# Optimization experiments

Hardware: AMD Instinct MI355X
Metric: run time of the kernel (lower is better)

## Reference

```python
import jax, jax.numpy as jnp
import numpy as np

N = 300000   # nodes
E = 600000   # edges
H = 128      # hidden_dim
L = 5        # num_layers
G = 8192     # graphs in batch
AV = 128     # atom feature vocab
BV = 8       # bond feature vocab
NAF = 9      # atom int features (OGB)
NBF = 3      # bond int features (OGB)
BN_EPS = 1e-5


def setup_inputs() -> dict:
    key = jax.random.key(0)
    ks = jax.random.split(key, 16)
    s = 0.05
    x = jax.random.randint(ks[0], (N, NAF), 0, 100, dtype=jnp.int32)
    edge_index = jax.random.randint(ks[1], (2, E), 0, N, dtype=jnp.int32)
    edge_attr = jax.random.randint(ks[2], (E, NBF), 0, 6, dtype=jnp.int32)
    batch = jnp.sort(jax.random.randint(ks[3], (N,), 0, G, dtype=jnp.int32))
    atom_emb = jax.random.normal(ks[4], (NAF, AV, H), dtype=jnp.float32) * s
    bond_emb = jax.random.normal(ks[5], (L, NBF, BV, H), dtype=jnp.float32) * s
    eps = jnp.zeros((L,), dtype=jnp.float32)  # GIN train_eps init 0
    w1 = jax.random.normal(ks[6], (L, H, H), dtype=jnp.float32) * s
    b1 = jnp.zeros((L, H), dtype=jnp.float32)
    bn1_g = jnp.ones((L, H), dtype=jnp.float32)
    bn1_b = jnp.zeros((L, H), dtype=jnp.float32)
    w2 = jax.random.normal(ks[7], (L, H, H), dtype=jnp.float32) * s
    b2 = jnp.zeros((L, H), dtype=jnp.float32)
    bn_g = jnp.ones((L, H), dtype=jnp.float32)
    bn_b = jnp.zeros((L, H), dtype=jnp.float32)
    cw1 = jax.random.normal(ks[8], (H, H), dtype=jnp.float32) * s
    cb1 = jnp.zeros((H,), dtype=jnp.float32)
    cw2 = jax.random.normal(ks[9], (H, 1), dtype=jnp.float32) * s
    cb2 = jnp.zeros((1,), dtype=jnp.float32)
    return dict(x=x, edge_index=edge_index, edge_attr=edge_attr, batch=batch,
                atom_emb=atom_emb, bond_emb=bond_emb, eps=eps,
                w1=w1, b1=b1, bn1_g=bn1_g, bn1_b=bn1_b, w2=w2, b2=b2,
                bn_g=bn_g, bn_b=bn_b, cw1=cw1, cb1=cb1, cw2=cw2, cb2=cb2)


def _bn(h, g, b):
    # BatchNorm1d in training mode: biased batch stats over nodes
    mu = h.mean(axis=0)
    var = h.var(axis=0)
    return g * (h - mu) * jax.lax.rsqrt(var + BN_EPS) + b


def reference(x, edge_index, edge_attr, batch, atom_emb, bond_emb, eps,
              w1, b1, bn1_g, bn1_b, w2, b2, bn_g, bn_b, cw1, cb1, cw2, cb2):
    seg = jax.ops.segment_sum
    # AtomEncoder: sum of per-feature embedding lookups -> [N, H]
    h = atom_emb[0][x[:, 0]]
    for f in range(1, NAF):
        h = h + atom_emb[f][x[:, f]]
    row, col = edge_index[0], edge_index[1]
    # in-degree of row used by scatter_reduce_(mean, include_self=True): divide by count+1
    deg = seg(jnp.ones((E,), dtype=h.dtype), row, num_segments=N)
    inv = 1.0 / (deg + 1.0)
    for l in range(L):
        # BondEncoder for this layer -> [E, H]
        be = (bond_emb[l, 0][edge_attr[:, 0]]
              + bond_emb[l, 1][edge_attr[:, 1]]
              + bond_emb[l, 2][edge_attr[:, 2]])
        # scatter mean (include_self=True over initial zeros): sum/(count+1)
        bond_agg = seg(be, row, num_segments=N) * inv[:, None]
        h_in = h + bond_agg
        # GINConv: sum-aggregate source feats at targets, (1+eps)*self + aggr, then MLP
        aggr = seg(h_in[row], col, num_segments=N)
        z = (1.0 + eps[l]) * h_in + aggr
        z = jax.nn.relu(_bn(z @ w1[l] + b1[l], bn1_g[l], bn1_b[l]))
        z = z @ w2[l] + b2[l]
        h = _bn(z, bn_g[l], bn_b[l])
        if l < L - 1:
            h = jax.nn.relu(h)  # dropout p=0 -> identity
    pooled = seg(h, batch, num_segments=G)  # global_add_pool -> [G, H]
    out = jax.nn.relu(pooled @ cw1 + cb1) @ cw2 + cb2  # [G, 1]
    return out.squeeze(-1)
```

## Files before the change

### kernel.cpp

```cpp
#include <hip/hip_runtime.h>
#include <cstdint>

#define NN 300000
#define NE 600000
#define HD 128
#define NL 5
#define NG 8192
#define AVOC 128
#define BVOC 8
#define NAF 9
#define NBF 3
#define BN_EPS 1e-5f

#define SCAN_B 2048
#define SCAN_NB ((NN + SCAN_B - 1) / SCAN_B)

#define G1ROWS 128
#define G1BLK ((NN + G1ROWS - 1) / G1ROWS)
#define GBM 256
#define GBLK ((NN + GBM - 1) / GBM)

typedef unsigned short u16;
typedef unsigned int u32;
typedef __attribute__((ext_vector_type(8))) short bf16x8;
typedef __attribute__((ext_vector_type(4))) float f32x4;

static __device__ __forceinline__ void atomAddF(float* p, float v) { unsafeAtomicAdd(p, v); }

static __device__ __forceinline__ float bf2f(u16 v) {
  union { u32 u; float f; } c; c.u = ((u32)v) << 16; return c.f;
}
static __device__ __forceinline__ u16 f2bf(float f) {
  union { float f; u32 u; } c; c.f = f;
  u32 u = c.u;
  return (u16)((u + 0x7FFFu + ((u >> 16) & 1u)) >> 16);
}
static __device__ __forceinline__ u32 cvtpk(float a, float b) {
  u32 r;
  asm("v_cvt_pk_bf16_f32 %0, %1, %2" : "=v"(r) : "v"(a), "v"(b));
  return r;
}
static __device__ __forceinline__ void unp8(uint4 p, float* v) {
  v[0] = bf2f((u16)(p.x & 0xffff)); v[1] = bf2f((u16)(p.x >> 16));
  v[2] = bf2f((u16)(p.y & 0xffff)); v[3] = bf2f((u16)(p.y >> 16));
  v[4] = bf2f((u16)(p.z & 0xffff)); v[5] = bf2f((u16)(p.z >> 16));
  v[6] = bf2f((u16)(p.w & 0xffff)); v[7] = bf2f((u16)(p.w >> 16));
}
static __device__ __forceinline__ uint4 pk8(const float* v) {
  uint4 p;
  p.x = ((u32)f2bf(v[1]) << 16) | f2bf(v[0]);
  p.y = ((u32)f2bf(v[3]) << 16) | f2bf(v[2]);
  p.z = ((u32)f2bf(v[5]) << 16) | f2bf(v[4]);
  p.w = ((u32)f2bf(v[7]) << 16) | f2bf(v[6]);
  return p;
}

static __device__ __forceinline__ void split8(const float* v, bf16x8& hi, bf16x8& lo) {
  union { u32 u[4]; bf16x8 h; } H, L;
  H.u[0] = cvtpk(v[0], v[1]); H.u[1] = cvtpk(v[2], v[3]);
  H.u[2] = cvtpk(v[4], v[5]); H.u[3] = cvtpk(v[6], v[7]);
  float r[8];
  r[0] = bf2f((u16)(H.u[0] & 0xffff)); r[1] = bf2f((u16)(H.u[0] >> 16));
  r[2] = bf2f((u16)(H.u[1] & 0xffff)); r[3] = bf2f((u16)(H.u[1] >> 16));
  r[4] = bf2f((u16)(H.u[2] & 0xffff)); r[5] = bf2f((u16)(H.u[2] >> 16));
  r[6] = bf2f((u16)(H.u[3] & 0xffff)); r[7] = bf2f((u16)(H.u[3] >> 16));
  L.u[0] = cvtpk(v[0] - r[0], v[1] - r[1]); L.u[1] = cvtpk(v[2] - r[2], v[3] - r[3]);
  L.u[2] = cvtpk(v[4] - r[4], v[5] - r[5]); L.u[3] = cvtpk(v[6] - r[6], v[7] - r[7]);
  hi = H.h; lo = L.h;
}

__global__ __launch_bounds__(256) void count_k(const int* __restrict__ ei,
    int* __restrict__ cnt_row, int* __restrict__ cnt_col) {
  int e = blockIdx.x * 256 + threadIdx.x;
  if (e >= NE) return;
  atomicAdd(&cnt_row[ei[e]], 1);
  atomicAdd(&cnt_col[ei[NE + e]], 1);
}

__global__ __launch_bounds__(256) void scan_block_k(int* __restrict__ P, int* __restrict__ bsum) {
  __shared__ int s[256];
  int b = blockIdx.x, t = threadIdx.x;
  int base = b * SCAN_B + t * 8;
  int v[8]; int ts = 0;
#pragma unroll
  for (int j = 0; j < 8; j++) { v[j] = (base + j < NN) ? P[base + j] : 0; ts += v[j]; }
  s[t] = ts;
  __syncthreads();
  for (int off = 1; off < 256; off <<= 1) {
    int tmp = 0;
    if (t >= off) tmp = s[t - off];
    __syncthreads();
    if (t >= off) s[t] += tmp;
    __syncthreads();
  }
  if (t == 255) bsum[b] = s[255];
  int run = (t == 0) ? 0 : s[t - 1];
#pragma unroll
  for (int j = 0; j < 8; j++) {
    if (base + j < NN) P[base + j] = run;
    run += v[j];
  }
}

__global__ __launch_bounds__(256) void scan_tops_k(int* __restrict__ bsum, int* __restrict__ totOut) {
  __shared__ int s[256];
  int t = threadIdx.x;
  s[t] = (t < SCAN_NB) ? bsum[t] : 0;
  __syncthreads();
  for (int off = 1; off < 256; off <<= 1) {
    int tmp = 0;
    if (t >= off) tmp = s[t - off];
    __syncthreads();
    if (t >= off) s[t] += tmp;
    __syncthreads();
  }
  if (t < SCAN_NB) bsum[t] = (t == 0) ? 0 : s[t - 1];
  if (t == 255) *totOut = s[255];
}

__global__ __launch_bounds__(256) void scan_add_k(int* __restrict__ P, const int* __restrict__ bsum) {
  int b = blockIdx.x, t = threadIdx.x;
  int off = bsum[b];
  int base = b * SCAN_B + t * 8;
#pragma unroll
  for (int j = 0; j < 8; j++)
    if (base + j < NN) P[base + j] += off;
}

__global__ __launch_bounds__(256) void fill_k(const int* __restrict__ ei,
    const int* __restrict__ ea,
    const int* __restrict__ ptr_row, const int* __restrict__ ptr_col,
    int* __restrict__ fillr, int* __restrict__ fillc,
    u16* __restrict__ adjc, int* __restrict__ adj_col) {
  int e = blockIdx.x * 256 + threadIdx.x;
  if (e >= NE) return;
  int r = ei[e], c = ei[NE + e];
  int a0 = ea[e * 3 + 0], a1 = ea[e * 3 + 1], a2 = ea[e * 3 + 2];
  int p1 = atomicAdd(&fillr[r], 1);
  adjc[ptr_row[r] + p1] = (u16)(a0 + (a1 << 3) + (a2 << 6));
  int p2 = atomicAdd(&fillc[c], 1);
  adj_col[ptr_col[c] + p2] = r;
}

__global__ __launch_bounds__(256) void inv_k(const int* __restrict__ ptr_row, float* __restrict__ inv) {
  int n = blockIdx.x * 256 + threadIdx.x;
  if (n < NN) inv[n] = 1.0f / ((float)(ptr_row[n + 1] - ptr_row[n]) + 1.0f);
}

__global__ __launch_bounds__(256) void gp_k(const int* __restrict__ batch, int* __restrict__ gp) {
  int g = blockIdx.x * 256 + threadIdx.x;
  if (g > NG) return;
  int lo = 0, hi = NN;
  while (lo < hi) { int mid = (lo + hi) >> 1; if (batch[mid] < g) lo = mid + 1; else hi = mid; }
  gp[g] = lo;
}

__global__ __launch_bounds__(256) void wsplit_k(const float* __restrict__ w1,
    const float* __restrict__ w2, u16* __restrict__ Wt_hi, u16* __restrict__ Wt_lo) {
  int m = blockIdx.x;
  const float* W = (m < NL) ? (w1 + (size_t)m * HD * HD) : (w2 + (size_t)(m - NL) * HD * HD);
  int t = threadIdx.x;
  for (int p = 0; p < 64; p++) {
    int o = p * 256 + t;
    int c = o >> 7, k = o & 127;
    float w = W[k * HD + c];
    u16 hi = f2bf(w);
    float lo = w - bf2f(hi);
    Wt_hi[(size_t)m * HD * HD + o] = hi;
    Wt_lo[(size_t)m * HD * HD + o] = f2bf(lo);
  }
}

__global__ __launch_bounds__(128) void cmb_k(const float* __restrict__ bond_emb,
    u16* __restrict__ cmb) {
  int b = blockIdx.x;
  int l = b >> 9, c = b & 511;
  int t = threadIdx.x;
  const float* be = bond_emb + (size_t)l * NBF * BVOC * HD;
  float v = be[(c & 7) * HD + t] + be[(BVOC + ((c >> 3) & 7)) * HD + t]
          + be[(2 * BVOC + (c >> 6)) * HD + t];
  cmb[(size_t)b * HD + t] = f2bf(v);
}


template<bool ENC>
__global__ __launch_bounds__(256) void bond_k(
    const u16* __restrict__ cmb, const int* __restrict__ ptr_row,
    const u16* __restrict__ adjc, const float* __restrict__ inv,
    const int* __restrict__ x, const float* __restrict__ emb,
    const u16* __restrict__ Z2, const float* __restrict__ stR,
    const float* __restrict__ bg, const float* __restrict__ bb_,
    u16* __restrict__ A) {
  __shared__ int sx[16 * NAF];
  __shared__ float sss[256];
  int t = threadIdx.x;
  int nb = blockIdx.x * 16;
  int n = nb + (t >> 4);
  int c8 = t & 15;
  if constexpr (ENC) {
    if (t < 16 * NAF && nb * NAF + t < NN * NAF) sx[t] = x[nb * NAF + t];
    __syncthreads();
  } else {
    if (t < 128) {
      float mean = stR[t] * (1.0f / NN);
      float var = stR[128 + t] * (1.0f / NN) - mean * mean;
      float sc = bg[t] * rsqrtf(var + BN_EPS);
      sss[t] = sc;
      sss[128 + t] = fmaf(-mean, sc, bb_[t]);
    }
    __syncthreads();
  }
  if (n >= NN) return;
  int beg = ptr_row[n], end = ptr_row[n + 1];
  float acc[8] = {0.f, 0.f, 0.f, 0.f, 0.f, 0.f, 0.f, 0.f};
  {
    int i = beg;
    int ca = (beg < end) ? (int)adjc[beg] : 0;
    int cb = (beg + 1 < end) ? (int)adjc[beg + 1] : 0;
    while (i + 1 < end) {
      uint4 pa = *(const uint4*)(cmb + ((size_t)ca << 7) + c8 * 8);
      uint4 pb = *(const uint4*)(cmb + ((size_t)cb << 7) + c8 * 8);
      i += 2;
      if (i < end)     ca = (int)adjc[i];
      if (i + 1 < end) cb = (int)adjc[i + 1];
      float va[8], vb[8];
      unp8(pa, va); unp8(pb, vb);
#pragma unroll
      for (int j = 0; j < 8; j++) acc[j] += va[j];
#pragma unroll
      for (int j = 0; j < 8; j++) acc[j] += vb[j];
    }
    if (i < end) {
      uint4 pa = *(const uint4*)(cmb + ((size_t)ca << 7) + c8 * 8);
      float va[8]; unp8(pa, va);
#pragma unroll
      for (int j = 0; j < 8; j++) acc[j] += va[j];
    }
  }
  float h[8];
  if constexpr (ENC) {
#pragma unroll
    for (int j = 0; j < 8; j++) h[j] = 0.f;
#pragma unroll
    for (int f = 0; f < NAF; f++) {
      int v = sx[(t >> 4) * NAF + f];
      const float* e = emb + ((size_t)(f * AVOC + v)) * HD + c8 * 8;
      float4 e0 = *(const float4*)e;
      float4 e1 = *(const float4*)(e + 4);
      h[0] += e0.x; h[1] += e0.y; h[2] += e0.z; h[3] += e0.w;
      h[4] += e1.x; h[5] += e1.y; h[6] += e1.z; h[7] += e1.w;
    }
  } else {
    uint4 p = *(const uint4*)(Z2 + (size_t)n * HD + c8 * 8);
    unp8(p, h);
#pragma unroll
    for (int j = 0; j < 8; j++)
      h[j] = fmaxf(fmaf(h[j], sss[c8 * 8 + j], sss[128 + c8 * 8 + j]), 0.f);
  }
  float iv = inv[n];
#pragma unroll
  for (int j = 0; j < 8; j++) h[j] = fmaf(acc[j], iv, h[j]);
  *(uint4*)(A + (size_t)n * HD + c8 * 8) = pk8(h);
}

__global__ __launch_bounds__(512, 4) void gemm1_aggr_k(
    const u16* __restrict__ A, const int* __restrict__ ptr_col,
    const int* __restrict__ adj_col, const float* __restrict__ eps, int lyr,
    const u16* __restrict__ Whi, const u16* __restrict__ Wlo,
    const float* __restrict__ bias, u16* __restrict__ Z1,
    float* __restrict__ stats) {
  __shared__ u16 sW[2 * HD * HD];
  const int tid = threadIdx.x;
#pragma unroll
  for (int p = 0; p < 4; p++) {
    int idx = tid + p * 512;
    int col = idx >> 4, k16 = idx & 15;
    uint4 vh = *(const uint4*)(Whi + idx * 8);
    uint4 vl = *(const uint4*)(Wlo + idx * 8);
    int so = (col << 7) + ((k16 << 3) ^ ((col & 7) << 3));
    *(uint4*)(sW + so) = vh;
    *(uint4*)(sW + HD * HD + so) = vl;
  }
  __syncthreads();

  const int bswz = (blockIdx.x & 7) * (G1BLK >> 3) + (blockIdx.x >> 3);

  const float se = 1.0f + eps[lyr];
  const int l = tid & 63, w = tid >> 6;
  const int lr = l & 15, lk = l >> 4;
  const int rw = bswz * G1ROWS + w * 16;
  const int gr = rw + lr;
  const int kb0 = lk * 8;

  float z[4][8];
#pragma unroll
  for (int ks = 0; ks < 4; ks++)
#pragma unroll
    for (int j = 0; j < 8; j++) z[ks][j] = 0.f;

  if (gr < NN) {
    const u16* ap = A + (size_t)gr * HD + kb0;
    uint4 s0 = *(const uint4*)(ap);
    uint4 s1 = *(const uint4*)(ap + 32);
    uint4 s2 = *(const uint4*)(ap + 64);
    uint4 s3 = *(const uint4*)(ap + 96);
    int beg = ptr_col[gr], end = ptr_col[gr + 1];
    {
      float v[8];
      unp8(s0, v);
#pragma unroll
      for (int j = 0; j < 8; j++) z[0][j] = v[j] * se;
      unp8(s1, v);
#pragma unroll
      for (int j = 0; j < 8; j++) z[1][j] = v[j] * se;
      unp8(s2, v);
#pragma unroll
      for (int j = 0; j < 8; j++) z[2][j] = v[j] * se;
      unp8(s3, v);
#pragma unroll
      for (int j = 0; j < 8; j++) z[3][j] = v[j] * se;
    }
    int i = beg;
    int srcA = (beg < end) ? adj_col[beg] : 0;
    int srcB = (beg + 1 < end) ? adj_col[beg + 1] : 0;
    while (i + 1 < end) {
      const u16* pa = A + (size_t)srcA * HD + kb0;
      const u16* pb = A + (size_t)srcB * HD + kb0;
      uint4 a0 = *(const uint4*)(pa);
      uint4 a1 = *(const uint4*)(pa + 32);
      uint4 a2 = *(const uint4*)(pa + 64);
      uint4 a3 = *(const uint4*)(pa + 96);
      uint4 b0 = *(const uint4*)(pb);
      uint4 b1 = *(const uint4*)(pb + 32);
      uint4 b2 = *(const uint4*)(pb + 64);
      uint4 b3 = *(const uint4*)(pb + 96);
      i += 2;
      if (i < end)     srcA = adj_col[i];
      if (i + 1 < end) srcB = adj_col[i + 1];
      float u[8];
      unp8(a0, u);
#pragma unroll
      for (int j = 0; j < 8; j++) z[0][j] += u[j];
      unp8(a1, u);
#pragma unroll
      for (int j = 0; j < 8; j++) z[1][j] += u[j];
      unp8(a2, u);
#pragma unroll
      for (int j = 0; j < 8; j++) z[2][j] += u[j];
      unp8(a3, u);
#pragma unroll
      for (int j = 0; j < 8; j++) z[3][j] += u[j];
      unp8(b0, u);
#pragma unroll
      for (int j = 0; j < 8; j++) z[0][j] += u[j];
      unp8(b1, u);
#pragma unroll
      for (int j = 0; j < 8; j++) z[1][j] += u[j];
      unp8(b2, u);
#pragma unroll
      for (int j = 0; j < 8; j++) z[2][j] += u[j];
      unp8(b3, u);
#pragma unroll
      for (int j = 0; j < 8; j++) z[3][j] += u[j];
    }
    if (i < end) {
      const u16* pa = A + (size_t)srcA * HD + kb0;
      uint4 a0 = *(const uint4*)(pa);
      uint4 a1 = *(const uint4*)(pa + 32);
      uint4 a2 = *(const uint4*)(pa + 64);
      uint4 a3 = *(const uint4*)(pa + 96);
      float u[8];
      unp8(a0, u);
#pragma unroll
      for (int j = 0; j < 8; j++) z[0][j] += u[j];
      unp8(a1, u);
#pragma unroll
      for (int j = 0; j < 8; j++) z[1][j] += u[j];
      unp8(a2, u);
#pragma unroll
      for (int j = 0; j < 8; j++) z[2][j] += u[j];
      unp8(a3, u);
#pragma unroll
      for (int j = 0; j < 8; j++) z[3][j] += u[j];
    }
  }

  bf16x8 ah[4], al[4];
#pragma unroll
  for (int ks = 0; ks < 4; ks++) split8(z[ks], ah[ks], al[ks]);

  f32x4 acc[8];
#pragma unroll
  for (int jt = 0; jt < 8; jt++) acc[jt] = (f32x4){0.f, 0.f, 0.f, 0.f};
#pragma unroll
  for (int ks = 0; ks < 4; ks++) {
    const int kb = ks * 32 + kb0;
#pragma unroll
    for (int jt = 0; jt < 8; jt++) {
      int col = jt * 16 + lr;
      int so = (col << 7) + (kb ^ ((col & 7) << 3));
      bf16x8 bh = *(const bf16x8*)(sW + so);
      bf16x8 bl = *(const bf16x8*)(sW + HD * HD + so);
      acc[jt] = __builtin_amdgcn_mfma_f32_16x16x32_bf16(ah[ks], bh, acc[jt], 0, 0, 0);
      acc[jt] = __builtin_amdgcn_mfma_f32_16x16x32_bf16(al[ks], bh, acc[jt], 0, 0, 0);
      acc[jt] = __builtin_amdgcn_mfma_f32_16x16x32_bf16(ah[ks], bl, acc[jt], 0, 0, 0);
    }
  }

  float bb[8];
#pragma unroll
  for (int jt = 0; jt < 8; jt++) bb[jt] = bias[jt * 16 + lr];
  float cs[8], cq[8];
#pragma unroll
  for (int jt = 0; jt < 8; jt++) { cs[jt] = 0.f; cq[jt] = 0.f; }
#pragma unroll
  for (int j = 0; j < 4; j++) {
    int gr2 = rw + lk * 4 + j;
    bool ok = gr2 < NN;
#pragma unroll
    for (int jt = 0; jt < 8; jt++) {
      float o = acc[jt][j] + bb[jt];
      if (ok) { cs[jt] += o; cq[jt] += o * o; }
      float on = __shfl_xor(o, 1);
      u32 pw = cvtpk(o, on);
      if (ok && !(l & 1))
        *(u32*)(Z1 + (size_t)gr2 * HD + jt * 16 + lr) = pw;
    }
  }
#pragma unroll
  for (int jt = 0; jt < 8; jt++) {
    cs[jt] += __shfl_xor(cs[jt], 16); cs[jt] += __shfl_xor(cs[jt], 32);
    cq[jt] += __shfl_xor(cq[jt], 16); cq[jt] += __shfl_xor(cq[jt], 32);
  }
  __syncthreads();
  float* sS = (float*)sW;
  if (lk == 0) {
#pragma unroll
    for (int jt = 0; jt < 8; jt++) {
      sS[w * HD + jt * 16 + lr] = cs[jt];
      sS[1024 + w * HD + jt * 16 + lr] = cq[jt];
    }
  }
  __syncthreads();
  if (tid < HD) {
    float s = 0.f, q = 0.f;
#pragma unroll
    for (int g = 0; g < 8; g++) { s += sS[g * HD + tid]; q += sS[1024 + g * HD + tid]; }
    atomAddF(&stats[tid], s);
    atomAddF(&stats[HD + tid], q);
  }
}

__global__ __launch_bounds__(512, 4) void gemm2_k(
    const u16* __restrict__ Z1, const float* __restrict__ stR,
    const float* __restrict__ g1, const float* __restrict__ b1_,
    const u16* __restrict__ Whi, const u16* __restrict__ Wlo,
    const float* __restrict__ bias, u16* __restrict__ Z2,
    float* __restrict__ stats) {
  __shared__ u16 sW[2 * HD * HD];
  __shared__ float sss[256];
  const int tid = threadIdx.x;
#pragma unroll
  for (int p = 0; p < 4; p++) {
    int idx = tid + p * 512;
    int col = idx >> 4, k16 = idx & 15;
    uint4 vh = *(const uint4*)(Whi + idx * 8);
    uint4 vl = *(const uint4*)(Wlo + idx * 8);
    int so = (col << 7) + ((k16 << 3) ^ ((col & 7) << 3));
    *(uint4*)(sW + so) = vh;
    *(uint4*)(sW + HD * HD + so) = vl;
  }
  if (tid < 128) {
    float mean = stR[tid] * (1.0f / NN);
    float var = stR[128 + tid] * (1.0f / NN) - mean * mean;
    float sc = g1[tid] * rsqrtf(var + BN_EPS);
    sss[tid] = sc;
    sss[128 + tid] = fmaf(-mean, sc, b1_[tid]);
  }
  __syncthreads();

  const int l = tid & 63, w = tid >> 6;
  const int lr = l & 15, lk = l >> 4;
  const int rw = blockIdx.x * GBM + w * 32;
  f32x4 acc[2][8];
#pragma unroll
  for (int i = 0; i < 2; i++)
#pragma unroll
    for (int j = 0; j < 8; j++) acc[i][j] = (f32x4){0.f, 0.f, 0.f, 0.f};

#pragma unroll
  for (int ks = 0; ks < 4; ks++) {
    const int kb = ks * 32 + lk * 8;
    bf16x8 ah[2], al[2];
#pragma unroll
    for (int i = 0; i < 2; i++) {
      int gr = rw + i * 16 + lr;
      uint4 p = make_uint4(0u, 0u, 0u, 0u);
      if (gr < NN) p = *(const uint4*)(Z1 + (size_t)gr * HD + kb);
      float v[8]; unp8(p, v);
#pragma unroll
      for (int j = 0; j < 8; j++)
        v[j] = fmaxf(fmaf(v[j], sss[kb + j], sss[128 + kb + j]), 0.f);
      split8(v, ah[i], al[i]);
    }
#pragma unroll
    for (int jt = 0; jt < 8; jt++) {
      int col = jt * 16 + lr;
      int so = (col << 7) + (kb ^ ((col & 7) << 3));
      bf16x8 bh = *(const bf16x8*)(sW + so);
      bf16x8 bl = *(const bf16x8*)(sW + HD * HD + so);
#pragma unroll
      for (int i = 0; i < 2; i++) {
        acc[i][jt] = __builtin_amdgcn_mfma_f32_16x16x32_bf16(ah[i], bh, acc[i][jt], 0, 0, 0);
        acc[i][jt] = __builtin_amdgcn_mfma_f32_16x16x32_bf16(al[i], bh, acc[i][jt], 0, 0, 0);
        acc[i][jt] = __builtin_amdgcn_mfma_f32_16x16x32_bf16(ah[i], bl, acc[i][jt], 0, 0, 0);
      }
    }
  }

  float bb[8];
#pragma unroll
  for (int jt = 0; jt < 8; jt++) bb[jt] = bias[jt * 16 + lr];
  float cs[8], cq[8];
#pragma unroll
  for (int jt = 0; jt < 8; jt++) { cs[jt] = 0.f; cq[jt] = 0.f; }
#pragma unroll
  for (int i = 0; i < 2; i++)
#pragma unroll
    for (int j = 0; j < 4; j++) {
      int gr = rw + i * 16 + lk * 4 + j;
      bool ok = gr < NN;
#pragma unroll
      for (int jt = 0; jt < 8; jt++) {
        float o = acc[i][jt][j] + bb[jt];
        if (ok) { cs[jt] += o; cq[jt] += o * o; }
        float on = __shfl_xor(o, 1);
        u32 pw = cvtpk(o, on);
        if (ok && !(l & 1))
          *(u32*)(Z2 + (size_t)gr * HD + jt * 16 + lr) = pw;
      }
    }
#pragma unroll
  for (int jt = 0; jt < 8; jt++) {
    cs[jt] += __shfl_xor(cs[jt], 16); cs[jt] += __shfl_xor(cs[jt], 32);
    cq[jt] += __shfl_xor(cq[jt], 16); cq[jt] += __shfl_xor(cq[jt], 32);
  }
  __syncthreads();
  float* sS = (float*)sW;
  if (lk == 0) {
#pragma unroll
    for (int jt = 0; jt < 8; jt++) {
      sS[w * HD + jt * 16 + lr] = cs[jt];
      sS[1024 + w * HD + jt * 16 + lr] = cq[jt];
    }
  }
  __syncthreads();
  if (tid < HD) {
    float s = 0.f, q = 0.f;
#pragma unroll
    for (int g = 0; g < 8; g++) { s += sS[g * HD + tid]; q += sS[1024 + g * HD + tid]; }
    atomAddF(&stats[tid], s);
    atomAddF(&stats[HD + tid], q);
  }
}

__global__ __launch_bounds__(128) void pool_final_k(const u16* __restrict__ Z2,
    const float* __restrict__ stR,
    const float* __restrict__ bg, const float* __restrict__ bb_,
    const int* __restrict__ gp,
    const float* __restrict__ cw1, const float* __restrict__ cb1,
    const float* __restrict__ cw2, const float* __restrict__ cb2,
    float* __restrict__ out) {
  __shared__ float sp[128];
  __shared__ float sh[128];
  int g = blockIdx.x, t = threadIdx.x;
  float mean = stR[t] * (1.0f / NN);
  float var = stR[128 + t] * (1.0f / NN) - mean * mean;
  float sc = bg[t] * rsqrtf(var + BN_EPS);
  float shf = fmaf(-mean, sc, bb_[t]);
  int beg = gp[g], end = gp[g + 1];
  float acc = 0.f;
  for (int n = beg; n < end; n++) acc += bf2f(Z2[(size_t)n * HD + t]);
  sp[t] = fmaf(acc, sc, (float)(end - beg) * shf);
  __syncthreads();
  float h1 = cb1[t];
#pragma unroll
  for (int k = 0; k < HD; k++) h1 = fmaf(sp[k], cw1[k * HD + t], h1);
  h1 = fmaxf(h1, 0.f);
  sh[t] = h1 * cw2[t];
  __syncthreads();
  for (int s = 64; s >= 1; s >>= 1) {
    if (t < s) sh[t] += sh[t + s];
    __syncthreads();
  }
  if (t == 0) out[g] = sh[0] + cb2[0];
}

extern "C" void kernel_launch(void* const* d_in, const int* in_sizes, int n_in,
                              void* d_out, int out_size, void* d_ws, size_t ws_size,
                              hipStream_t stream) {
  const int*   x        = (const int*)d_in[0];
  const int*   ei       = (const int*)d_in[1];
  const int*   ea       = (const int*)d_in[2];
  const int*   batch    = (const int*)d_in[3];
  const float* atom_emb = (const float*)d_in[4];
  const float* bond_emb = (const float*)d_in[5];
  const float* eps      = (const float*)d_in[6];
  const float* w1       = (const float*)d_in[7];
  const float* b1       = (const float*)d_in[8];
  const float* bn1_g    = (const float*)d_in[9];
  const float* bn1_b    = (const float*)d_in[10];
  const float* w2       = (const float*)d_in[11];
  const float* b2       = (const float*)d_in[12];
  const float* bn_g     = (const float*)d_in[13];
  const float* bn_b     = (const float*)d_in[14];
  const float* cw1      = (const float*)d_in[15];
  const float* cb1      = (const float*)d_in[16];
  const float* cw2      = (const float*)d_in[17];
  const float* cb2      = (const float*)d_in[18];
  float* out = (float*)d_out;

  const size_t NH = (size_t)NN * HD;
  float* ws = (float*)d_ws;
  float* stats   = ws;
  int*   ptr_row = (int*)(ws + 5 * 1024);
  int*   ptr_col = ptr_row + (NN + 1);
  u16*   adjc    = (u16*)(ptr_col + (NN + 1));
  int*   adj_col = (int*)adjc + NE;
  int*   gp      = adj_col + NE;
  float* inv     = (float*)(gp + (NG + 1));
  size_t off = 5 * 1024 + 2 * (size_t)(NN + 1) + 2 * (size_t)NE + (NG + 1) + NN;
  off = (off + 3) & ~(size_t)3;
  float* B = ws + off;
  u16*   Z1 = (u16*)B;
  u16*   Z2 = Z1 + NH;
  u16*   A  = (u16*)(B + NH);
  u16*   Wt_hi = A + NH;
  u16*   Wt_lo = Wt_hi + 10 * HD * HD;
  u16*   cmb   = Wt_lo + 10 * HD * HD;
  int* fillr = (int*)B;
  int* fillc = fillr + NN;
  int* bsums = fillc + NN;

  const int nb_node = (NN + 15) / 16;
  const int nb_n256 = (NN + 255) / 256;
  const int nb_e    = (NE + 255) / 256;

  hipMemsetAsync(stats, 0, 5 * 1024 * sizeof(float), stream);
  hipMemsetAsync(ptr_row, 0, 2 * (NN + 1) * sizeof(int), stream);
  hipMemsetAsync(fillr, 0, 2 * NN * sizeof(int), stream);

  count_k<<<nb_e, 256, 0, stream>>>(ei, ptr_row, ptr_col);
  scan_block_k<<<SCAN_NB, 256, 0, stream>>>(ptr_row, bsums);
  scan_tops_k<<<1, 256, 0, stream>>>(bsums, &ptr_row[NN]);
  scan_add_k<<<SCAN_NB, 256, 0, stream>>>(ptr_row, bsums);
  scan_block_k<<<SCAN_NB, 256, 0, stream>>>(ptr_col, bsums);
  scan_tops_k<<<1, 256, 0, stream>>>(bsums, &ptr_col[NN]);
  scan_add_k<<<SCAN_NB, 256, 0, stream>>>(ptr_col, bsums);
  inv_k<<<nb_n256, 256, 0, stream>>>(ptr_row, inv);
  fill_k<<<nb_e, 256, 0, stream>>>(ei, ea, ptr_row, ptr_col, fillr, fillc, adjc, adj_col);
  wsplit_k<<<2 * NL, 256, 0, stream>>>(w1, w2, Wt_hi, Wt_lo);
  cmb_k<<<NL * 512, 128, 0, stream>>>(bond_emb, cmb);
  gp_k<<<(NG + 1 + 255) / 256, 256, 0, stream>>>(batch, gp);

  for (int l = 0; l < NL; l++) {
    const u16* cl = cmb + (size_t)l * 512 * HD;
    float* st = stats + (size_t)l * 1024;
    if (l == 0) {
      bond_k<true><<<nb_node, 256, 0, stream>>>(cl, ptr_row, adjc, inv,
          x, atom_emb, nullptr, nullptr, nullptr, nullptr, A);
    } else {
      bond_k<false><<<nb_node, 256, 0, stream>>>(cl, ptr_row, adjc, inv,
          nullptr, nullptr, Z2, stats + (size_t)(l - 1) * 1024 + 512,
          bn_g + (size_t)(l - 1) * HD, bn_b + (size_t)(l - 1) * HD, A);
    }
    gemm1_aggr_k<<<G1BLK, 512, 0, stream>>>(A, ptr_col, adj_col, eps, l,
        Wt_hi + (size_t)l * HD * HD, Wt_lo + (size_t)l * HD * HD,
        b1 + (size_t)l * HD, Z1, st);
    gemm2_k<<<GBLK, 512, 0, stream>>>(Z1, st,
        bn1_g + (size_t)l * HD, bn1_b + (size_t)l * HD,
        Wt_hi + (size_t)(NL + l) * HD * HD, Wt_lo + (size_t)(NL + l) * HD * HD,
        b2 + (size_t)l * HD, Z2, st + 512);
  }

  pool_final_k<<<NG, 128, 0, stream>>>(Z2, stats + 4 * 1024 + 512,
      bn_g + 4 * HD, bn_b + 4 * HD, gp, cw1, cb1, cw2, cb2, out);
}
```

Before: 1.331 ms.

## Precompute bond aggregation for all layers in one pass and stream per-layer

Adds a kernel that walks each node's row adjacency once and accumulates the combined bond embeddings for all five layers, storing five bf16 [N,H] aggregates in workspace. Per-layer bond kernels then become pure streaming elementwise kernels that read the precomputed aggregate instead of re-walking the CSR. This removes four repeated irregular CSR walks, at the cost of writing and re-reading about 5*N*H bf16 of extra traffic. It falls back to the old path if the workspace is too small. It also removes the block-index swizzle in gemm1_aggr_k.

New measurement: 1.331 ms. Within noise of the previous version (-0.0%).

```diff
diff --git a/kernel.cpp b/kernel.cpp
--- a/kernel.cpp
+++ b/kernel.cpp
@@ -180,6 +180,49 @@
   float v = be[(c & 7) * HD + t] + be[(BVOC + ((c >> 3) & 7)) * HD + t]
           + be[(2 * BVOC + (c >> 6)) * HD + t];
   cmb[(size_t)b * HD + t] = f2bf(v);
+}
+
+__global__ __launch_bounds__(256) void baggall_k(const u16* __restrict__ cmb,
+    const int* __restrict__ ptr_row, const u16* __restrict__ adjc,
+    u16* __restrict__ bagg) {
+  int t = threadIdx.x;
+  int n = blockIdx.x * 16 + (t >> 4);
+  int c8 = t & 15;
+  if (n >= NN) return;
+  int beg = ptr_row[n], end = ptr_row[n + 1];
+  float ac[5][8];
+#pragma unroll
+  for (int l = 0; l < 5; l++)
+#pragma unroll
+    for (int j = 0; j < 8; j++) ac[l][j] = 0.f;
+  int c = (beg < end) ? (int)adjc[beg] : 0;
+  for (int i = beg; i < end; i++) {
+    uint4 p0 = *(const uint4*)(cmb + (((size_t)(0 * 512 + c)) << 7) + c8 * 8);
+    uint4 p1 = *(const uint4*)(cmb + (((size_t)(1 * 512 + c)) << 7) + c8 * 8);
+    uint4 p2 = *(const uint4*)(cmb + (((size_t)(2 * 512 + c)) << 7) + c8 * 8);
+    uint4 p3 = *(const uint4*)(cmb + (((size_t)(3 * 512 + c)) << 7) + c8 * 8);
+    uint4 p4 = *(const uint4*)(cmb + (((size_t)(4 * 512 + c)) << 7) + c8 * 8);
+    if (i + 1 < end) c = (int)adjc[i + 1];
+    float v[8];
+    unp8(p0, v);
+#pragma unroll
+    for (int j = 0; j < 8; j++) ac[0][j] += v[j];
+    unp8(p1, v);
+#pragma unroll
+    for (int j = 0; j < 8; j++) ac[1][j] += v[j];
+    unp8(p2, v);
+#pragma unroll
+    for (int j = 0; j < 8; j++) ac[2][j] += v[j];
+    unp8(p3, v);
+#pragma unroll
+    for (int j = 0; j < 8; j++) ac[3][j] += v[j];
+    unp8(p4, v);
+#pragma unroll
+    for (int j = 0; j < 8; j++) ac[4][j] += v[j];
+  }
+#pragma unroll
+  for (int l = 0; l < 5; l++)
+    *(uint4*)(bagg + (size_t)l * NN * HD + (size_t)n * HD + c8 * 8) = pk8(ac[l]);
 }
 
 
@@ -263,6 +306,69 @@
   *(uint4*)(A + (size_t)n * HD + c8 * 8) = pk8(h);
 }
 
+__global__ __launch_bounds__(256) void enc_stream_k(
+    const u16* __restrict__ bagg0, const float* __restrict__ inv,
+    const int* __restrict__ x, const float* __restrict__ emb,
+    u16* __restrict__ A) {
+  __shared__ int sx[16 * NAF];
+  int t = threadIdx.x;
+  int nb = blockIdx.x * 16;
+  int n = nb + (t >> 4);
+  int c8 = t & 15;
+  if (t < 16 * NAF && nb * NAF + t < NN * NAF) sx[t] = x[nb * NAF + t];
+  __syncthreads();
+  if (n >= NN) return;
+  uint4 pb = *(const uint4*)(bagg0 + (size_t)n * HD + c8 * 8);
+  float h[8];
+#pragma unroll
+  for (int j = 0; j < 8; j++) h[j] = 0.f;
+#pragma unroll
+  for (int f = 0; f < NAF; f++) {
+    int v = sx[(t >> 4) * NAF + f];
+    const float* e = emb + ((size_t)(f * AVOC + v)) * HD + c8 * 8;
+    float4 e0 = *(const float4*)e;
+    float4 e1 = *(const float4*)(e + 4);
+    h[0] += e0.x; h[1] += e0.y; h[2] += e0.z; h[3] += e0.w;
+    h[4] += e1.x; h[5] += e1.y; h[6] += e1.z; h[7] += e1.w;
+  }
+  float g[8]; unp8(pb, g);
+  float iv = inv[n];
+#pragma unroll
+  for (int j = 0; j < 8; j++) h[j] = fmaf(g[j], iv, h[j]);
+  *(uint4*)(A + (size_t)n * HD + c8 * 8) = pk8(h);
+}
+
+__global__ __launch_bounds__(256) void bond_stream_k(
+    const u16* __restrict__ Z2, const u16* __restrict__ BAGG,
+    const float* __restrict__ inv, const float* __restrict__ stR,
+    const float* __restrict__ bg, const float* __restrict__ bb_,
+    u16* __restrict__ A) {
+  __shared__ float sss[256];
+  int t = threadIdx.x;
+  if (t < 128) {
+    float mean = stR[t] * (1.0f / NN);
+    float var = stR[128 + t] * (1.0f / NN) - mean * mean;
+    float sc = bg[t] * rsqrtf(var + BN_EPS);
+    sss[t] = sc;
+    sss[128 + t] = fmaf(-mean, sc, bb_[t]);
+  }
+  __syncthreads();
+  int gid = blockIdx.x * 256 + t;
+  if (gid >= NN * 16) return;
+  int n = gid >> 4, c8 = gid & 15;
+  uint4 pz = *(const uint4*)(Z2 + (size_t)n * HD + c8 * 8);
+  uint4 pb = *(const uint4*)(BAGG + (size_t)n * HD + c8 * 8);
+  float h[8], g[8];
+  unp8(pz, h); unp8(pb, g);
+  float iv = inv[n];
+#pragma unroll
+  for (int j = 0; j < 8; j++) {
+    h[j] = fmaxf(fmaf(h[j], sss[c8 * 8 + j], sss[128 + c8 * 8 + j]), 0.f);
+    h[j] = fmaf(g[j], iv, h[j]);
+  }
+  *(uint4*)(A + (size_t)n * HD + c8 * 8) = pk8(h);
+}
+
 __global__ __launch_bounds__(512, 4) void gemm1_aggr_k(
     const u16* __restrict__ A, const int* __restrict__ ptr_col,
     const int* __restrict__ adj_col, const float* __restrict__ eps, int lyr,
@@ -283,12 +389,10 @@
   }
   __syncthreads();
 
-  const int bswz = (blockIdx.x & 7) * (G1BLK >> 3) + (blockIdx.x >> 3);
-
   const float se = 1.0f + eps[lyr];
   const int l = tid & 63, w = tid >> 6;
   const int lr = l & 15, lk = l >> 4;
-  const int rw = bswz * G1ROWS + w * 16;
+  const int rw = blockIdx.x * G1ROWS + w * 16;
   const int gr = rw + lr;
   const int kb0 = lk * 8;
 
@@ -638,11 +742,15 @@
   u16*   Wt_hi = A + NH;
   u16*   Wt_lo = Wt_hi + 10 * HD * HD;
   u16*   cmb   = Wt_lo + 10 * HD * HD;
+  u16*   bagg  = cmb + (size_t)NL * 512 * HD;
+  const size_t need = (size_t)((char*)(bagg + (size_t)NL * NH) - (char*)d_ws);
+  const bool fast = ws_size >= need;
   int* fillr = (int*)B;
   int* fillc = fillr + NN;
   int* bsums = fillc + NN;
 
   const int nb_node = (NN + 15) / 16;
+  const int nb_n16  = (int)(((size_t)NN * 16 + 255) / 256);
   const int nb_n256 = (NN + 255) / 256;
   const int nb_e    = (NE + 255) / 256;
 
@@ -661,18 +769,27 @@
   fill_k<<<nb_e, 256, 0, stream>>>(ei, ea, ptr_row, ptr_col, fillr, fillc, adjc, adj_col);
   wsplit_k<<<2 * NL, 256, 0, stream>>>(w1, w2, Wt_hi, Wt_lo);
   cmb_k<<<NL * 512, 128, 0, stream>>>(bond_emb, cmb);
+  if (fast) baggall_k<<<nb_node, 256, 0, stream>>>(cmb, ptr_row, adjc, bagg);
   gp_k<<<(NG + 1 + 255) / 256, 256, 0, stream>>>(batch, gp);
 
   for (int l = 0; l < NL; l++) {
     const u16* cl = cmb + (size_t)l * 512 * HD;
     float* st = stats + (size_t)l * 1024;
     if (l == 0) {
-      bond_k<true><<<nb_node, 256, 0, stream>>>(cl, ptr_row, adjc, inv,
-          x, atom_emb, nullptr, nullptr, nullptr, nullptr, A);
+      if (fast)
+        enc_stream_k<<<nb_node, 256, 0, stream>>>(bagg, inv, x, atom_emb, A);
+      else
+        bond_k<true><<<nb_node, 256, 0, stream>>>(cl, ptr_row, adjc, inv,
+            x, atom_emb, nullptr, nullptr, nullptr, nullptr, A);
     } else {
-      bond_k<false><<<nb_node, 256, 0, stream>>>(cl, ptr_row, adjc, inv,
-          nullptr, nullptr, Z2, stats + (size_t)(l - 1) * 1024 + 512,
-          bn_g + (size_t)(l - 1) * HD, bn_b + (size_t)(l - 1) * HD, A);
+      if (fast)
+        bond_stream_k<<<nb_n16, 256, 0, stream>>>(Z2, bagg + (size_t)l * NH, inv,
+            stats + (size_t)(l - 1) * 1024 + 512,
+            bn_g + (size_t)(l - 1) * HD, bn_b + (size_t)(l - 1) * HD, A);
+      else
+        bond_k<false><<<nb_node, 256, 0, stream>>>(cl, ptr_row, adjc, inv,
+            nullptr, nullptr, Z2, stats + (size_t)(l - 1) * 1024 + 512,
+            bn_g + (size_t)(l - 1) * HD, bn_b + (size_t)(l - 1) * HD, A);
     }
     gemm1_aggr_k<<<G1BLK, 512, 0, stream>>>(A, ptr_col, adj_col, eps, l,
         Wt_hi + (size_t)l * HD * HD, Wt_lo + (size_t)l * HD * HD,
```
